# Kernel optimization log

Hardware: AMD Instinct MI355X
Metric: run time of the kernel (lower is better)

Reference implementation:

```python
import jax, jax.numpy as jnp
import numpy as np

N, T, D, E1 = 64, 32, 128, 128
EPS = 1e-6


def _mlp(x, W1, b1, W2, b2):
    # Linear -> ReLU -> (Dropout: identity in eval) -> Linear
    return jnp.maximum(x @ W1 + b1, 0.0) @ W2 + b2


def _forward(x_time, x_news,
             it_W1, it_b1, it_W2, it_b2,
             inw_W1, inw_b1, inw_W2, inw_b2,
             t2n_W1, t2n_b1, t2n_W2, t2n_b2,
             n2t_W1, n2t_b1, n2t_W2, n2t_b2,
             f_W1, f_b1, f_W2, f_b2,
             theta_t, theta_n):
    xt = x_time.reshape(-1, D)   # [NT, D]
    xn = x_news.reshape(-1, D)   # [NT, D]

    # incidence-matrix candidates, each [NT, E1]
    H_time = xt @ _mlp(xt.T, it_W1, it_b1, it_W2, it_b2)
    H_news = xn @ _mlp(xn.T, inw_W1, inw_b1, inw_W2, inw_b2)
    H_t2n = xt @ _mlp(xn.T, t2n_W1, t2n_b1, t2n_W2, t2n_b2)
    H_n2t = xn @ _mlp(xt.T, n2t_W1, n2t_b1, n2t_W2, n2t_b2)

    H = _mlp(jnp.concatenate([H_time, H_news, H_t2n, H_n2t], axis=1),
             f_W1, f_b1, f_W2, f_b2)  # [NT, E1]

    # column-wise standardization (torch.std is unbiased -> ddof=1) + softmax over nodes
    H = (H - H.mean(axis=0, keepdims=True)) / (H.std(axis=0, ddof=1, keepdims=True) + EPS)
    H = jax.nn.softmax(H, axis=0)

    # pairwise Jensen-Shannon divergence between columns of H -> [E1, E1]
    logH = jnp.log(H)
    M = (H[:, :, None] + H[:, None, :]) * 0.5          # [NT, E1, E1]
    kl_pm = jnp.sum(H[:, :, None] * (logH[:, :, None] - jnp.log(M)), axis=0)  # KL(P||M)
    # KL(Q||M)[i,j] == KL(P||M)[j,i] since M is symmetric in (i,j)
    jsd = (kl_pm + kl_pm.T) * 0.5

    jm = jsd.mean(axis=0)                               # [E1]
    njm = (jm - jm.mean()) / (jm.std(ddof=1) + EPS)
    w = jax.nn.softmax(njm)                             # diagonal of hyperedge weight W

    # Hypergraph conv with residual: x + elu(H @ diag(w) @ H.T @ x @ theta)
    # reassociated (exactly equal math) to avoid the O((NT)^2) intermediate
    Hw = H * w[None, :]                                 # [NT, E1]
    xt = xt + jax.nn.elu(Hw @ (H.T @ (xt @ theta_t)))
    xn = xn + jax.nn.elu(Hw @ (H.T @ (xn @ theta_n)))

    return xt.reshape(N, T, D), xn.reshape(N, T, D)


def setup_inputs() -> dict:
    key = jax.random.key(0)
    ks = iter(jax.random.split(key, 32))
    NT = N * T

    def lin(i, o):
        return (jax.random.normal(next(ks), (i, o), jnp.float32) / np.float32(np.sqrt(i)))

    inp = {
        "x_time": jax.random.normal(next(ks), (N, T, D), jnp.float32),
        "x_news": jax.random.normal(next(ks), (N, T, D), jnp.float32),
    }
    for pre in ["it", "inw", "t2n", "n2t"]:
        inp[pre + "_W1"] = lin(NT, E1)
        inp[pre + "_b1"] = jnp.zeros((E1,), jnp.float32)
        inp[pre + "_W2"] = lin(E1, E1)
        inp[pre + "_b2"] = jnp.zeros((E1,), jnp.float32)
    inp["f_W1"] = lin(4 * E1, E1)
    inp["f_b1"] = jnp.zeros((E1,), jnp.float32)
    inp["f_W2"] = lin(E1, E1)
    inp["f_b2"] = jnp.zeros((E1,), jnp.float32)
    # HypergraphConvolution uses torch.randn init for theta
    inp["theta_t"] = jax.random.normal(next(ks), (D, D), jnp.float32)
    inp["theta_n"] = jax.random.normal(next(ks), (D, D), jnp.float32)
    return inp


def reference(x_time, x_news,
              it_W1, it_b1, it_W2, it_b2,
              inw_W1, inw_b1, inw_W2, inw_b2,
              t2n_W1, t2n_b1, t2n_W2, t2n_b2,
              n2t_W1, n2t_b1, n2t_W2, n2t_b2,
              f_W1, f_b1, f_W2, f_b2,
              theta_t, theta_n):
    return _forward(x_time, x_news,
                    it_W1, it_b1, it_W2, it_b2,
                    inw_W1, inw_b1, inw_W2, inw_b2,
                    t2n_W1, t2n_b1, t2n_W2, t2n_b2,
                    n2t_W1, n2t_b1, n2t_W2, n2t_b2,
                    f_W1, f_b1, f_W2, f_b2,
                    theta_t, theta_n)
```

## Files before the change

### kernel.cpp

```cpp
#include <hip/hip_runtime.h>
#include <hip/hip_bf16.h>
#include <math.h>

#define NTOT 2048
#define DIM  128
#define MSPLIT 8
#define ZSPLIT 8
#define JT 16
#define JNC 128
#define JNSPLIT 8

struct P4 { const float* p[4]; };

__global__ __launch_bounds__(256) void gk_mlp1t(P4 X, P4 W1, float* __restrict__ Gs) {
  int k = blockIdx.z;
  int m0 = (blockIdx.x & 3) * 32;
  int e0 = (blockIdx.x >> 2) * 32;
  int split = blockIdx.y;
  int n0 = split * (NTOT / MSPLIT);
  const float* Xp = X.p[k];
  const float* Wp = W1.p[k];
  __shared__ float Xs[32][36], Ws[32][36];
  int tid = threadIdx.x;
  int lr = tid >> 3;
  int lc = (tid & 7) * 4;
  int tx = tid & 15, ty = tid >> 4;
  float a00 = 0.f, a01 = 0.f, a10 = 0.f, a11 = 0.f;
  long g0 = (long)(n0 + lr) * DIM;
  float4 xv = *(const float4*)(Xp + g0 + m0 + lc);
  float4 wv = *(const float4*)(Wp + g0 + e0 + lc);
  for (int nb = 0; nb < NTOT / MSPLIT; nb += 32) {
    *(float4*)&Xs[lr][lc] = xv;
    *(float4*)&Ws[lr][lc] = wv;
    __syncthreads();
    if (nb + 32 < NTOT / MSPLIT) {
      long gn = (long)(n0 + nb + 32 + lr) * DIM;
      xv = *(const float4*)(Xp + gn + m0 + lc);
      wv = *(const float4*)(Wp + gn + e0 + lc);
    }
    #pragma unroll
    for (int nn = 0; nn < 32; ++nn) {
      float x0 = Xs[nn][2*ty], x1 = Xs[nn][2*ty+1];
      float w0 = Ws[nn][2*tx], w1 = Ws[nn][2*tx+1];
      a00 += x0 * w0; a01 += x0 * w1;
      a10 += x1 * w0; a11 += x1 * w1;
    }
    __syncthreads();
  }
  float* Gk = Gs + ((long)k * MSPLIT + split) * 16384;
  int m = m0 + 2 * ty, e = e0 + 2 * tx;
  Gk[m * DIM + e]           = a00;
  Gk[m * DIM + e + 1]       = a01;
  Gk[(m + 1) * DIM + e]     = a10;
  Gk[(m + 1) * DIM + e + 1] = a11;
}

__global__ __launch_bounds__(256) void gk_mab(const float* __restrict__ Gs, P4 B1, P4 W2, P4 B2,
                                              const float* __restrict__ fW1, float* __restrict__ AB) {
  int m = blockIdx.x;
  int e = threadIdx.x & 127;
  int half = threadIdx.x >> 7;
  int k0 = half, k1 = half + 2;
  __shared__ float rk[4][DIM];
  __shared__ float mk[4][DIM];
  {
    const float* G0 = Gs + (long)k0 * MSPLIT * 16384 + m * DIM + e;
    const float* G1 = Gs + (long)k1 * MSPLIT * 16384 + m * DIM + e;
    float s0 = 0.f, s1 = 0.f;
    #pragma unroll
    for (int s = 0; s < MSPLIT; ++s) { s0 += G0[s * 16384]; s1 += G1[s * 16384]; }
    rk[k0][e] = fmaxf(s0 + B1.p[k0][e], 0.f);
    rk[k1][e] = fmaxf(s1 + B1.p[k1][e], 0.f);
  }
  __syncthreads();
  {
    const float* Wa = W2.p[k0];
    const float* Wb = W2.p[k1];
    float a0 = B2.p[k0][e], a1 = B2.p[k1][e];
    #pragma unroll 8
    for (int j = 0; j < DIM; ++j) {
      a0 += rk[k0][j] * Wa[j * DIM + e];
      a1 += rk[k1][j] * Wb[j * DIM + e];
    }
    mk[k0][e] = a0;
    mk[k1][e] = a1;
  }
  __syncthreads();
  const float* Ma = mk[half];
  const float* Mb = mk[half + 2];
  const float* W0 = fW1 + (half == 0 ? 0 : 128) * DIM;
  const float* W1p = fW1 + (half == 0 ? 256 : 384) * DIM;
  float acc = 0.f;
  #pragma unroll 8
  for (int j = 0; j < DIM; ++j)
    acc += Ma[j] * W0[j * DIM + e] + Mb[j] * W1p[j * DIM + e];
  AB[(long)half * 16384 + m * DIM + e] = acc;
}

__global__ __launch_bounds__(256) void gk_h12t(const float* __restrict__ xt, const float* __restrict__ xn,
                                               const float* __restrict__ AB, const float* __restrict__ fb1,
                                               const float* __restrict__ fW2, const float* __restrict__ fb2,
                                               float* __restrict__ HrawT) {
  int n0 = blockIdx.x * 8;
  int e  = threadIdx.x & 127;
  int rr = (threadIdx.x >> 7) << 2;
  __shared__ float stT[DIM][8], snT[DIM][8], h1T[DIM][8];
  {
    int c = threadIdx.x & 31, rq = threadIdx.x >> 5;
    const float* xtr = xt + (long)(n0 + rq) * DIM;
    const float* xnr = xn + (long)(n0 + rq) * DIM;
    #pragma unroll
    for (int i = 0; i < 4; ++i) {
      int d = c + 32 * i;
      stT[d][rq] = xtr[d];
      snT[d][rq] = xnr[d];
    }
  }
  __syncthreads();
  float4 acc1 = make_float4(0.f, 0.f, 0.f, 0.f);
  #pragma unroll 8
  for (int k = 0; k < DIM; ++k) {
    float a = AB[k * DIM + e];
    float b = AB[16384 + k * DIM + e];
    const float4 xv = *(const float4*)&stT[k][rr];
    const float4 nv = *(const float4*)&snT[k][rr];
    acc1.x += xv.x * a + nv.x * b;
    acc1.y += xv.y * a + nv.y * b;
    acc1.z += xv.z * a + nv.z * b;
    acc1.w += xv.w * a + nv.w * b;
  }
  float b1v = fb1[e];
  float4 h1;
  h1.x = fmaxf(acc1.x + b1v, 0.f);
  h1.y = fmaxf(acc1.y + b1v, 0.f);
  h1.z = fmaxf(acc1.z + b1v, 0.f);
  h1.w = fmaxf(acc1.w + b1v, 0.f);
  *(float4*)&h1T[e][rr] = h1;
  __syncthreads();
  float4 acc2 = make_float4(0.f, 0.f, 0.f, 0.f);
  #pragma unroll 8
  for (int j = 0; j < DIM; ++j) {
    float wv = fW2[j * DIM + e];
    const float4 hv = *(const float4*)&h1T[j][rr];
    acc2.x += hv.x * wv;
    acc2.y += hv.y * wv;
    acc2.z += hv.z * wv;
    acc2.w += hv.w * wv;
  }
  float b2v = fb2[e];
  float4 o;
  o.x = acc2.x + b2v; o.y = acc2.y + b2v; o.z = acc2.z + b2v; o.w = acc2.w + b2v;
  *(float4*)&HrawT[(long)e * NTOT + n0 + rr] = o;
}

__global__ __launch_bounds__(256) void colsoft_k(const float* __restrict__ HrawT,
                                                 float* __restrict__ HTp, float* __restrict__ Ecol,
                                                 float* __restrict__ Gacc) {
  int e = blockIdx.x;
  int t = threadIdx.x;
  if (e == 0 && t < DIM) Gacc[t] = 0.f;
  __shared__ float sa[4], sb[4], sc[4];
  float v[8];
  float sum = 0.f, sq = 0.f, mx = -3.4e38f;
  #pragma unroll
  for (int r = 0; r < 8; ++r) {
    float x = HrawT[(long)e * NTOT + t + 256 * r];
    v[r] = x;
    sum += x; sq += x * x; mx = fmaxf(mx, x);
  }
  #pragma unroll
  for (int o = 32; o > 0; o >>= 1) {
    sum += __shfl_down(sum, o);
    sq  += __shfl_down(sq, o);
    mx   = fmaxf(mx, __shfl_down(mx, o));
  }
  if ((t & 63) == 0) { int w = t >> 6; sa[w] = sum; sb[w] = sq; sc[w] = mx; }
  __syncthreads();
  sum = sa[0] + sa[1] + sa[2] + sa[3];
  sq  = sb[0] + sb[1] + sb[2] + sb[3];
  mx  = fmaxf(fmaxf(sc[0], sc[1]), fmaxf(sc[2], sc[3]));
  float mean = sum * (1.f / NTOT);
  float var  = (sq - sum * mean) * (1.f / (NTOT - 1));
  float ia   = 1.f / (sqrtf(fmaxf(var, 0.f)) + 1e-6f);
  float smax = (mx - mean) * ia;
  __syncthreads();

  float den = 0.f;
  #pragma unroll
  for (int r = 0; r < 8; ++r) {
    float s = (v[r] - mean) * ia - smax;
    v[r] = s;
    den += __expf(s);
  }
  #pragma unroll
  for (int o = 32; o > 0; o >>= 1) den += __shfl_down(den, o);
  if ((t & 63) == 0) sa[t >> 6] = den;
  __syncthreads();
  den = sa[0] + sa[1] + sa[2] + sa[3];
  float logden = __logf(den);
  float invden = 1.f / den;
  __syncthreads();

  float ent = 0.f;
  #pragma unroll
  for (int r = 0; r < 8; ++r) {
    float s = v[r];
    float pv = __expf(s) * invden;
    HTp[(long)e * NTOT + t + 256 * r] = pv;
    ent += pv * (s - logden);
  }
  #pragma unroll
  for (int o = 32; o > 0; o >>= 1) ent += __shfl_down(ent, o);
  if ((t & 63) == 0) sa[t >> 6] = ent;
  __syncthreads();
  if (t == 0) Ecol[e] = sa[0] + sa[1] + sa[2] + sa[3];
}

__global__ __launch_bounds__(256) void jsd_tile(const float* __restrict__ HTp,
                                                float* __restrict__ g) {
  int b = blockIdx.x;
  int bi = 0, rem = b;
  while (rem >= 8 - bi) { rem -= 8 - bi; ++bi; }
  int bj = bi + rem;
  int n0 = blockIdx.y * (NTOT / JNSPLIT);

  __shared__ float Ti[JT][JNC + 2];
  __shared__ float Tj[JT][JNC + 2];
  __shared__ float red[JT][JT + 1];

  int tid = threadIdx.x;
  int ti = tid >> 4, tj = tid & 15;
  bool active = (bi != bj) || (ti < tj);
  float acc = 0.f;

  int lc = tid >> 4;
  int ln = (tid & 15) * 8;

  for (int c = 0; c < NTOT / JNSPLIT; c += JNC) {
    const float* si = HTp + (long)(bi * JT + lc) * NTOT + n0 + c + ln;
    const float* sj = HTp + (long)(bj * JT + lc) * NTOT + n0 + c + ln;
    #pragma unroll
    for (int r = 0; r < 8; ++r) Ti[lc][ln + r] = si[r];
    #pragma unroll
    for (int r = 0; r < 8; ++r) Tj[lc][ln + r] = sj[r];
    __syncthreads();
    if (active) {
      #pragma unroll 4
      for (int n = 0; n < JNC; ++n) {
        float s = Ti[ti][n] + Tj[tj][n];
        acc += s * __logf(fmaxf(0.5f * s, 1e-38f));
      }
    }
    __syncthreads();
  }

  red[ti][tj] = active ? acc : 0.f;
  __syncthreads();
  if (tid < JT) {
    float s = 0.f;
    #pragma unroll
    for (int j = 0; j < JT; ++j) s += red[tid][j];
    atomicAdd(&g[bi * JT + tid], -s);
  } else if (tid < 2 * JT) {
    int c2 = tid - JT;
    float s = 0.f;
    #pragma unroll
    for (int i = 0; i < JT; ++i) s += red[i][c2];
    atomicAdd(&g[bj * JT + c2], -s);
  }
}

__global__ __launch_bounds__(256) void xz_k(const float* __restrict__ HTp, const float* __restrict__ xt,
                                            const float* __restrict__ xn, float* __restrict__ Xzs) {
  int bt = blockIdx.z;
  const float* x = bt ? xn : xt;
  int split = blockIdx.y;
  float* C = Xzs + ((long)bt * ZSPLIT + split) * 16384;
  int e0 = (blockIdx.x & 3) * 32, d0 = (blockIdx.x >> 2) * 32;
  int n0 = split * (NTOT / ZSPLIT);
  __shared__ float As[32][33], Bs[32][36];
  int tid = threadIdx.x, col = tid & 31, row = tid >> 5;
  int lr = tid >> 3, lc4 = (tid & 7) * 4;
  int tx = tid & 15, ty = tid >> 4;
  float a00 = 0.f, a01 = 0.f, a10 = 0.f, a11 = 0.f;
  float pa[4]; float4 pb;
  #pragma unroll
  for (int r = 0; r < 4; ++r) pa[r] = HTp[(long)(e0 + row + r * 8) * NTOT + n0 + col];
  pb = *(const float4*)(x + (long)(n0 + lr) * DIM + d0 + lc4);
  for (int nb = 0; nb < NTOT / ZSPLIT; nb += 32) {
    #pragma unroll
    for (int r = 0; r < 4; ++r) As[col][row + r * 8] = pa[r];
    *(float4*)&Bs[lr][lc4] = pb;
    __syncthreads();
    if (nb + 32 < NTOT / ZSPLIT) {
      #pragma unroll
      for (int r = 0; r < 4; ++r)
        pa[r] = HTp[(long)(e0 + row + r * 8) * NTOT + n0 + nb + 32 + col];
      pb = *(const float4*)(x + (long)(n0 + nb + 32 + lr) * DIM + d0 + lc4);
    }
    #pragma unroll
    for (int nn = 0; nn < 32; ++nn) {
      float e0v = As[nn][2*ty], e1v = As[nn][2*ty+1];
      float d0v = Bs[nn][2*tx], d1v = Bs[nn][2*tx+1];
      a00 += e0v * d0v; a01 += e0v * d1v;
      a10 += e1v * d0v; a11 += e1v * d1v;
    }
    __syncthreads();
  }
  int e = e0 + 2 * ty, d = d0 + 2 * tx;
  C[e * DIM + d]           = a00;
  C[e * DIM + d + 1]       = a01;
  C[(e + 1) * DIM + d]     = a10;
  C[(e + 1) * DIM + d + 1] = a11;
}

__global__ __launch_bounds__(128) void zs_k(const float* __restrict__ Xzs, const float* __restrict__ thT,
                                            const float* __restrict__ thN, const float* __restrict__ g,
                                            const float* __restrict__ Ecol, float* __restrict__ Zw) {
  int e = blockIdx.x, d = threadIdx.x, bt = blockIdx.y;
  __shared__ float s2[2];
  __shared__ float swv;
  int t = d;
  float ec = Ecol[t];
  float v = ec;
  #pragma unroll
  for (int o = 32; o > 0; o >>= 1) v += __shfl_down(v, o);
  if ((t & 63) == 0) s2[t >> 6] = v;
  __syncthreads();
  float S = s2[0] + s2[1];
  __syncthreads();
  float jm = (g[t] + 126.f * ec + S) * (1.0f / 256.0f);
  v = jm;
  #pragma unroll
  for (int o = 32; o > 0; o >>= 1) v += __shfl_down(v, o);
  if ((t & 63) == 0) s2[t >> 6] = v;
  __syncthreads();
  float mean = (s2[0] + s2[1]) * (1.0f / 128.0f);
  __syncthreads();
  float dv = jm - mean;
  v = dv * dv;
  #pragma unroll
  for (int o = 32; o > 0; o >>= 1) v += __shfl_down(v, o);
  if ((t & 63) == 0) s2[t >> 6] = v;
  __syncthreads();
  float var = (s2[0] + s2[1]) * (1.0f / 127.0f);
  float njm = dv / (sqrtf(var) + 1e-6f);
  __syncthreads();
  v = njm;
  #pragma unroll
  for (int o = 32; o > 0; o >>= 1) v = fmaxf(v, __shfl_down(v, o));
  if ((t & 63) == 0) s2[t >> 6] = v;
  __syncthreads();
  float mx = fmaxf(s2[0], s2[1]);
  float ex = __expf(njm - mx);
  __syncthreads();
  v = ex;
  #pragma unroll
  for (int o = 32; o > 0; o >>= 1) v += __shfl_down(v, o);
  if ((t & 63) == 0) s2[t >> 6] = v;
  __syncthreads();
  if (t == e) swv = ex / (s2[0] + s2[1]);
  __syncthreads();
  float we = swv;

  const float* src = Xzs + (long)bt * ZSPLIT * 16384 + e * DIM + d;
  const float* th = bt ? thN : thT;
  __shared__ float s[DIM];
  float xv = 0.f;
  #pragma unroll
  for (int sp = 0; sp < ZSPLIT; ++sp) xv += src[sp * 16384];
  s[d] = xv;
  __syncthreads();
  float acc = 0.f;
  #pragma unroll 8
  for (int k = 0; k < DIM; ++k) acc += s[k] * th[(long)k * DIM + d];
  Zw[bt * 16384 + e * DIM + d] = acc * we;
}

__global__ __launch_bounds__(256) void uk_t(const float* __restrict__ HTp, const float* __restrict__ Zw,
                                            const float* __restrict__ xt, const float* __restrict__ xn,
                                            float* __restrict__ out) {
  int bt = blockIdx.z;
  const float* x = bt ? xn : xt;
  const float* B = Zw + bt * 16384;
  float* o = out + (long)bt * NTOT * DIM;
  int d0 = blockIdx.x * 32, n0 = blockIdx.y * 32;
  __shared__ float As[32][33], Bs[32][36];
  int tid = threadIdx.x, col = tid & 31, row = tid >> 5;
  int lr = tid >> 3, lc4 = (tid & 7) * 4;
  int tx = tid & 15, ty = tid >> 4;
  float a00 = 0.f, a01 = 0.f, a10 = 0.f, a11 = 0.f;
  float pa[4]; float4 pb;
  #pragma unroll
  for (int r = 0; r < 4; ++r) pa[r] = HTp[(long)(row + r * 8) * NTOT + n0 + col];
  pb = *(const float4*)(B + (long)lr * DIM + d0 + lc4);
  for (int eb = 0; eb < DIM; eb += 32) {
    #pragma unroll
    for (int r = 0; r < 4; ++r) As[col][row + r * 8] = pa[r];
    *(float4*)&Bs[lr][lc4] = pb;
    __syncthreads();
    if (eb + 32 < DIM) {
      #pragma unroll
      for (int r = 0; r < 4; ++r)
        pa[r] = HTp[(long)(eb + 32 + row + r * 8) * NTOT + n0 + col];
      pb = *(const float4*)(B + (long)(eb + 32 + lr) * DIM + d0 + lc4);
    }
    #pragma unroll
    for (int ee = 0; ee < 32; ++ee) {
      float x0 = As[2*ty][ee], x1 = As[2*ty+1][ee];
      float b0 = Bs[ee][2*tx], b1 = Bs[ee][2*tx+1];
      a00 += x0 * b0; a01 += x0 * b1;
      a10 += x1 * b0; a11 += x1 * b1;
    }
    __syncthreads();
  }
  int n = n0 + 2 * ty, d = d0 + 2 * tx;
  long i0 = (long)n * DIM + d, i1 = i0 + DIM;
  float e00 = a00 > 0.f ? a00 : expm1f(a00);
  float e01 = a01 > 0.f ? a01 : expm1f(a01);
  float e10 = a10 > 0.f ? a10 : expm1f(a10);
  float e11 = a11 > 0.f ? a11 : expm1f(a11);
  o[i0]     = x[i0]     + e00;
  o[i0 + 1] = x[i0 + 1] + e01;
  o[i1]     = x[i1]     + e10;
  o[i1 + 1] = x[i1 + 1] + e11;
}

extern "C" void kernel_launch(void* const* d_in, const int* in_sizes, int n_in,
                              void* d_out, int out_size, void* d_ws, size_t ws_size,
                              hipStream_t stream) {
  const float* xt = (const float*)d_in[0];
  const float* xn = (const float*)d_in[1];
  const float *W1[4], *b1[4], *W2[4], *b2[4];
  for (int k = 0; k < 4; ++k) {
    W1[k] = (const float*)d_in[2 + 4*k];
    b1[k] = (const float*)d_in[3 + 4*k];
    W2[k] = (const float*)d_in[4 + 4*k];
    b2[k] = (const float*)d_in[5 + 4*k];
  }
  const float* fW1 = (const float*)d_in[18];
  const float* fb1 = (const float*)d_in[19];
  const float* fW2 = (const float*)d_in[20];
  const float* fb2 = (const float*)d_in[21];
  const float* thT = (const float*)d_in[22];
  const float* thN = (const float*)d_in[23];

  float* ws    = (float*)d_ws;
  float* Gacc  = ws;
  float* Ecol  = ws + 128;
  float* Zw    = ws + 384;
  float* Xzs   = ws + 33152;
  float* Gs    = ws + 295296;
  float* AB    = ws + 885120;
  float* HrawT = ws + 917888;
  float* HTp   = ws + 1180032;

  float* out = (float*)d_out;

  P4 Xs  = {{xt, xn, xn, xt}};
  P4 W1s = {{W1[0], W1[1], W1[2], W1[3]}};
  P4 B1s = {{b1[0], b1[1], b1[2], b1[3]}};
  P4 W2s = {{W2[0], W2[1], W2[2], W2[3]}};
  P4 B2s = {{b2[0], b2[1], b2[2], b2[3]}};

  gk_mlp1t<<<dim3(16, MSPLIT, 4), 256, 0, stream>>>(Xs, W1s, Gs);
  gk_mab  <<<128, 256, 0, stream>>>(Gs, B1s, W2s, B2s, fW1, AB);
  gk_h12t <<<256, 256, 0, stream>>>(xt, xn, AB, fb1, fW2, fb2, HrawT);

  colsoft_k<<<DIM, 256, 0, stream>>>(HrawT, HTp, Ecol, Gacc);

  jsd_tile<<<dim3(36, JNSPLIT), 256, 0, stream>>>(HTp, Gacc);

  xz_k<<<dim3(16, ZSPLIT, 2), 256, 0, stream>>>(HTp, xt, xn, Xzs);
  zs_k<<<dim3(128, 2), 128, 0, stream>>>(Xzs, thT, thN, Gacc, Ecol, Zw);
  uk_t<<<dim3(4, 64, 2), 256, 0, stream>>>(HTp, Zw, xt, xn, out);

  (void)in_sizes; (void)n_in; (void)out_size; (void)ws_size;
}
```

Measured before the change: 183.8 us.

## Fuse all pipeline stages into one cooperative persistent kernel with grid syncs

Replaces the eight separate kernel launches with a single cooperative kernel of 512 blocks that runs every stage in sequence and separates the stages with grid-wide barriers. Stage work is remapped onto the fixed block count, which doubles the JSD and Xz split factors and halves the per-block rows in the H projection. The aim is to remove per-launch overhead and the gaps between the many small dependent kernels. In exchange, grid.sync costs are added, and stages with fewer tiles than blocks leave some blocks idle. The design also depends on all 512 blocks fitting at once, which launch_bounds(256,2) is meant to allow.

Measured after the change: 527.2 us. 187% more time.

```diff
diff --git a/kernel.cpp b/kernel.cpp
--- a/kernel.cpp
+++ b/kernel.cpp
@@ -1,429 +1,413 @@
 #include <hip/hip_runtime.h>
-#include <hip/hip_bf16.h>
+#include <hip/hip_cooperative_groups.h>
 #include <math.h>
+
+namespace cg = cooperative_groups;
 
 #define NTOT 2048
 #define DIM  128
 #define MSPLIT 8
-#define ZSPLIT 8
+#define ZSPLIT 16
 #define JT 16
 #define JNC 128
-#define JNSPLIT 8
-
-struct P4 { const float* p[4]; };
-
-__global__ __launch_bounds__(256) void gk_mlp1t(P4 X, P4 W1, float* __restrict__ Gs) {
-  int k = blockIdx.z;
-  int m0 = (blockIdx.x & 3) * 32;
-  int e0 = (blockIdx.x >> 2) * 32;
-  int split = blockIdx.y;
-  int n0 = split * (NTOT / MSPLIT);
-  const float* Xp = X.p[k];
-  const float* Wp = W1.p[k];
-  __shared__ float Xs[32][36], Ws[32][36];
-  int tid = threadIdx.x;
-  int lr = tid >> 3;
-  int lc = (tid & 7) * 4;
-  int tx = tid & 15, ty = tid >> 4;
-  float a00 = 0.f, a01 = 0.f, a10 = 0.f, a11 = 0.f;
-  long g0 = (long)(n0 + lr) * DIM;
-  float4 xv = *(const float4*)(Xp + g0 + m0 + lc);
-  float4 wv = *(const float4*)(Wp + g0 + e0 + lc);
-  for (int nb = 0; nb < NTOT / MSPLIT; nb += 32) {
-    *(float4*)&Xs[lr][lc] = xv;
-    *(float4*)&Ws[lr][lc] = wv;
-    __syncthreads();
-    if (nb + 32 < NTOT / MSPLIT) {
-      long gn = (long)(n0 + nb + 32 + lr) * DIM;
-      xv = *(const float4*)(Xp + gn + m0 + lc);
-      wv = *(const float4*)(Wp + gn + e0 + lc);
-    }
-    #pragma unroll
-    for (int nn = 0; nn < 32; ++nn) {
-      float x0 = Xs[nn][2*ty], x1 = Xs[nn][2*ty+1];
-      float w0 = Ws[nn][2*tx], w1 = Ws[nn][2*tx+1];
-      a00 += x0 * w0; a01 += x0 * w1;
-      a10 += x1 * w0; a11 += x1 * w1;
-    }
-    __syncthreads();
-  }
-  float* Gk = Gs + ((long)k * MSPLIT + split) * 16384;
-  int m = m0 + 2 * ty, e = e0 + 2 * tx;
-  Gk[m * DIM + e]           = a00;
-  Gk[m * DIM + e + 1]       = a01;
-  Gk[(m + 1) * DIM + e]     = a10;
-  Gk[(m + 1) * DIM + e + 1] = a11;
-}
-
-__global__ __launch_bounds__(256) void gk_mab(const float* __restrict__ Gs, P4 B1, P4 W2, P4 B2,
-                                              const float* __restrict__ fW1, float* __restrict__ AB) {
-  int m = blockIdx.x;
-  int e = threadIdx.x & 127;
-  int half = threadIdx.x >> 7;
-  int k0 = half, k1 = half + 2;
-  __shared__ float rk[4][DIM];
-  __shared__ float mk[4][DIM];
-  {
-    const float* G0 = Gs + (long)k0 * MSPLIT * 16384 + m * DIM + e;
-    const float* G1 = Gs + (long)k1 * MSPLIT * 16384 + m * DIM + e;
-    float s0 = 0.f, s1 = 0.f;
-    #pragma unroll
-    for (int s = 0; s < MSPLIT; ++s) { s0 += G0[s * 16384]; s1 += G1[s * 16384]; }
-    rk[k0][e] = fmaxf(s0 + B1.p[k0][e], 0.f);
-    rk[k1][e] = fmaxf(s1 + B1.p[k1][e], 0.f);
-  }
-  __syncthreads();
-  {
-    const float* Wa = W2.p[k0];
-    const float* Wb = W2.p[k1];
-    float a0 = B2.p[k0][e], a1 = B2.p[k1][e];
-    #pragma unroll 8
-    for (int j = 0; j < DIM; ++j) {
-      a0 += rk[k0][j] * Wa[j * DIM + e];
-      a1 += rk[k1][j] * Wb[j * DIM + e];
-    }
-    mk[k0][e] = a0;
-    mk[k1][e] = a1;
-  }
-  __syncthreads();
-  const float* Ma = mk[half];
-  const float* Mb = mk[half + 2];
-  const float* W0 = fW1 + (half == 0 ? 0 : 128) * DIM;
-  const float* W1p = fW1 + (half == 0 ? 256 : 384) * DIM;
-  float acc = 0.f;
-  #pragma unroll 8
-  for (int j = 0; j < DIM; ++j)
-    acc += Ma[j] * W0[j * DIM + e] + Mb[j] * W1p[j * DIM + e];
-  AB[(long)half * 16384 + m * DIM + e] = acc;
-}
-
-__global__ __launch_bounds__(256) void gk_h12t(const float* __restrict__ xt, const float* __restrict__ xn,
-                                               const float* __restrict__ AB, const float* __restrict__ fb1,
-                                               const float* __restrict__ fW2, const float* __restrict__ fb2,
-                                               float* __restrict__ HrawT) {
-  int n0 = blockIdx.x * 8;
-  int e  = threadIdx.x & 127;
-  int rr = (threadIdx.x >> 7) << 2;
-  __shared__ float stT[DIM][8], snT[DIM][8], h1T[DIM][8];
-  {
-    int c = threadIdx.x & 31, rq = threadIdx.x >> 5;
-    const float* xtr = xt + (long)(n0 + rq) * DIM;
-    const float* xnr = xn + (long)(n0 + rq) * DIM;
-    #pragma unroll
-    for (int i = 0; i < 4; ++i) {
-      int d = c + 32 * i;
-      stT[d][rq] = xtr[d];
-      snT[d][rq] = xnr[d];
-    }
-  }
-  __syncthreads();
-  float4 acc1 = make_float4(0.f, 0.f, 0.f, 0.f);
-  #pragma unroll 8
-  for (int k = 0; k < DIM; ++k) {
-    float a = AB[k * DIM + e];
-    float b = AB[16384 + k * DIM + e];
-    const float4 xv = *(const float4*)&stT[k][rr];
-    const float4 nv = *(const float4*)&snT[k][rr];
-    acc1.x += xv.x * a + nv.x * b;
-    acc1.y += xv.y * a + nv.y * b;
-    acc1.z += xv.z * a + nv.z * b;
-    acc1.w += xv.w * a + nv.w * b;
-  }
-  float b1v = fb1[e];
-  float4 h1;
-  h1.x = fmaxf(acc1.x + b1v, 0.f);
-  h1.y = fmaxf(acc1.y + b1v, 0.f);
-  h1.z = fmaxf(acc1.z + b1v, 0.f);
-  h1.w = fmaxf(acc1.w + b1v, 0.f);
-  *(float4*)&h1T[e][rr] = h1;
-  __syncthreads();
-  float4 acc2 = make_float4(0.f, 0.f, 0.f, 0.f);
-  #pragma unroll 8
-  for (int j = 0; j < DIM; ++j) {
-    float wv = fW2[j * DIM + e];
-    const float4 hv = *(const float4*)&h1T[j][rr];
-    acc2.x += hv.x * wv;
-    acc2.y += hv.y * wv;
-    acc2.z += hv.z * wv;
-    acc2.w += hv.w * wv;
-  }
-  float b2v = fb2[e];
-  float4 o;
-  o.x = acc2.x + b2v; o.y = acc2.y + b2v; o.z = acc2.z + b2v; o.w = acc2.w + b2v;
-  *(float4*)&HrawT[(long)e * NTOT + n0 + rr] = o;
-}
-
-__global__ __launch_bounds__(256) void colsoft_k(const float* __restrict__ HrawT,
-                                                 float* __restrict__ HTp, float* __restrict__ Ecol,
-                                                 float* __restrict__ Gacc) {
-  int e = blockIdx.x;
-  int t = threadIdx.x;
-  if (e == 0 && t < DIM) Gacc[t] = 0.f;
-  __shared__ float sa[4], sb[4], sc[4];
-  float v[8];
-  float sum = 0.f, sq = 0.f, mx = -3.4e38f;
-  #pragma unroll
-  for (int r = 0; r < 8; ++r) {
-    float x = HrawT[(long)e * NTOT + t + 256 * r];
-    v[r] = x;
-    sum += x; sq += x * x; mx = fmaxf(mx, x);
-  }
-  #pragma unroll
-  for (int o = 32; o > 0; o >>= 1) {
-    sum += __shfl_down(sum, o);
-    sq  += __shfl_down(sq, o);
-    mx   = fmaxf(mx, __shfl_down(mx, o));
-  }
-  if ((t & 63) == 0) { int w = t >> 6; sa[w] = sum; sb[w] = sq; sc[w] = mx; }
-  __syncthreads();
-  sum = sa[0] + sa[1] + sa[2] + sa[3];
-  sq  = sb[0] + sb[1] + sb[2] + sb[3];
-  mx  = fmaxf(fmaxf(sc[0], sc[1]), fmaxf(sc[2], sc[3]));
-  float mean = sum * (1.f / NTOT);
-  float var  = (sq - sum * mean) * (1.f / (NTOT - 1));
-  float ia   = 1.f / (sqrtf(fmaxf(var, 0.f)) + 1e-6f);
-  float smax = (mx - mean) * ia;
-  __syncthreads();
-
-  float den = 0.f;
-  #pragma unroll
-  for (int r = 0; r < 8; ++r) {
-    float s = (v[r] - mean) * ia - smax;
-    v[r] = s;
-    den += __expf(s);
-  }
-  #pragma unroll
-  for (int o = 32; o > 0; o >>= 1) den += __shfl_down(den, o);
-  if ((t & 63) == 0) sa[t >> 6] = den;
-  __syncthreads();
-  den = sa[0] + sa[1] + sa[2] + sa[3];
-  float logden = __logf(den);
-  float invden = 1.f / den;
-  __syncthreads();
-
-  float ent = 0.f;
-  #pragma unroll
-  for (int r = 0; r < 8; ++r) {
-    float s = v[r];
-    float pv = __expf(s) * invden;
-    HTp[(long)e * NTOT + t + 256 * r] = pv;
-    ent += pv * (s - logden);
-  }
-  #pragma unroll
-  for (int o = 32; o > 0; o >>= 1) ent += __shfl_down(ent, o);
-  if ((t & 63) == 0) sa[t >> 6] = ent;
-  __syncthreads();
-  if (t == 0) Ecol[e] = sa[0] + sa[1] + sa[2] + sa[3];
-}
-
-__global__ __launch_bounds__(256) void jsd_tile(const float* __restrict__ HTp,
-                                                float* __restrict__ g) {
-  int b = blockIdx.x;
+#define JNSPLIT 16
+#define NBLK 512
+
+struct KArgs {
+  const float* X[4];
+  const float* W1[4]; const float* B1[4];
+  const float* W2[4]; const float* B2[4];
+  const float *xt, *xn, *fW1, *fb1, *fW2, *fb2, *thT, *thN;
+  float *Gacc, *Ecol, *Zw, *Xzs, *Gs, *AB, *HrawT, *HTp, *out;
+};
+
+struct SMem {
+  union {
+    struct { float Xs[32][36], Ws[32][36]; } g1;
+    struct { float rk[4][DIM], mk[4][DIM]; } g2;
+    struct { float xT[DIM][4], nT[DIM][4], h1[DIM][4]; } g3;
+    struct { float sa[4], sb[4], sc[4]; } g4;
+    struct { float Ti[JT][JNC + 2], Tj[JT][JNC + 2], red[JT][JT + 1]; } g5;
+    struct { float As[32][33], Bs[32][36]; } g6;
+    struct { float s[DIM]; } g7;
+  };
+};
+
+__device__ __forceinline__ void jsd_body(SMem& sm, int j, const KArgs& A) {
+  int b = j % 36, ny = j / 36;
   int bi = 0, rem = b;
   while (rem >= 8 - bi) { rem -= 8 - bi; ++bi; }
   int bj = bi + rem;
-  int n0 = blockIdx.y * (NTOT / JNSPLIT);
-
-  __shared__ float Ti[JT][JNC + 2];
-  __shared__ float Tj[JT][JNC + 2];
-  __shared__ float red[JT][JT + 1];
-
+  int n0 = ny * (NTOT / JNSPLIT);
   int tid = threadIdx.x;
   int ti = tid >> 4, tj = tid & 15;
   bool active = (bi != bj) || (ti < tj);
+  int lc = tid >> 4, ln = (tid & 15) * 8;
+  __syncthreads();
+  const float* si = A.HTp + (long)(bi * JT + lc) * NTOT + n0 + ln;
+  const float* sj = A.HTp + (long)(bj * JT + lc) * NTOT + n0 + ln;
+  #pragma unroll
+  for (int r = 0; r < 8; ++r) sm.g5.Ti[lc][ln + r] = si[r];
+  #pragma unroll
+  for (int r = 0; r < 8; ++r) sm.g5.Tj[lc][ln + r] = sj[r];
+  __syncthreads();
   float acc = 0.f;
-
-  int lc = tid >> 4;
-  int ln = (tid & 15) * 8;
-
-  for (int c = 0; c < NTOT / JNSPLIT; c += JNC) {
-    const float* si = HTp + (long)(bi * JT + lc) * NTOT + n0 + c + ln;
-    const float* sj = HTp + (long)(bj * JT + lc) * NTOT + n0 + c + ln;
-    #pragma unroll
-    for (int r = 0; r < 8; ++r) Ti[lc][ln + r] = si[r];
-    #pragma unroll
-    for (int r = 0; r < 8; ++r) Tj[lc][ln + r] = sj[r];
-    __syncthreads();
-    if (active) {
-      #pragma unroll 4
-      for (int n = 0; n < JNC; ++n) {
-        float s = Ti[ti][n] + Tj[tj][n];
-        acc += s * __logf(fmaxf(0.5f * s, 1e-38f));
-      }
-    }
-    __syncthreads();
-  }
-
-  red[ti][tj] = active ? acc : 0.f;
+  if (active) {
+    #pragma unroll 4
+    for (int n = 0; n < JNC; ++n) {
+      float s = sm.g5.Ti[ti][n] + sm.g5.Tj[tj][n];
+      acc += s * __logf(fmaxf(0.5f * s, 1e-38f));
+    }
+  }
+  sm.g5.red[ti][tj] = active ? acc : 0.f;
   __syncthreads();
   if (tid < JT) {
     float s = 0.f;
     #pragma unroll
-    for (int j = 0; j < JT; ++j) s += red[tid][j];
-    atomicAdd(&g[bi * JT + tid], -s);
+    for (int q = 0; q < JT; ++q) s += sm.g5.red[tid][q];
+    atomicAdd(&A.Gacc[bi * JT + tid], -s);
   } else if (tid < 2 * JT) {
     int c2 = tid - JT;
     float s = 0.f;
     #pragma unroll
-    for (int i = 0; i < JT; ++i) s += red[i][c2];
-    atomicAdd(&g[bj * JT + c2], -s);
+    for (int i = 0; i < JT; ++i) s += sm.g5.red[i][c2];
+    atomicAdd(&A.Gacc[bj * JT + c2], -s);
   }
 }
 
-__global__ __launch_bounds__(256) void xz_k(const float* __restrict__ HTp, const float* __restrict__ xt,
-                                            const float* __restrict__ xn, float* __restrict__ Xzs) {
-  int bt = blockIdx.z;
-  const float* x = bt ? xn : xt;
-  int split = blockIdx.y;
-  float* C = Xzs + ((long)bt * ZSPLIT + split) * 16384;
-  int e0 = (blockIdx.x & 3) * 32, d0 = (blockIdx.x >> 2) * 32;
-  int n0 = split * (NTOT / ZSPLIT);
-  __shared__ float As[32][33], Bs[32][36];
-  int tid = threadIdx.x, col = tid & 31, row = tid >> 5;
-  int lr = tid >> 3, lc4 = (tid & 7) * 4;
-  int tx = tid & 15, ty = tid >> 4;
-  float a00 = 0.f, a01 = 0.f, a10 = 0.f, a11 = 0.f;
-  float pa[4]; float4 pb;
-  #pragma unroll
-  for (int r = 0; r < 4; ++r) pa[r] = HTp[(long)(e0 + row + r * 8) * NTOT + n0 + col];
-  pb = *(const float4*)(x + (long)(n0 + lr) * DIM + d0 + lc4);
-  for (int nb = 0; nb < NTOT / ZSPLIT; nb += 32) {
-    #pragma unroll
-    for (int r = 0; r < 4; ++r) As[col][row + r * 8] = pa[r];
-    *(float4*)&Bs[lr][lc4] = pb;
-    __syncthreads();
-    if (nb + 32 < NTOT / ZSPLIT) {
-      #pragma unroll
-      for (int r = 0; r < 4; ++r)
-        pa[r] = HTp[(long)(e0 + row + r * 8) * NTOT + n0 + nb + 32 + col];
-      pb = *(const float4*)(x + (long)(n0 + nb + 32 + lr) * DIM + d0 + lc4);
-    }
-    #pragma unroll
-    for (int nn = 0; nn < 32; ++nn) {
-      float e0v = As[nn][2*ty], e1v = As[nn][2*ty+1];
-      float d0v = Bs[nn][2*tx], d1v = Bs[nn][2*tx+1];
-      a00 += e0v * d0v; a01 += e0v * d1v;
-      a10 += e1v * d0v; a11 += e1v * d1v;
-    }
-    __syncthreads();
-  }
-  int e = e0 + 2 * ty, d = d0 + 2 * tx;
-  C[e * DIM + d]           = a00;
-  C[e * DIM + d + 1]       = a01;
-  C[(e + 1) * DIM + d]     = a10;
-  C[(e + 1) * DIM + d + 1] = a11;
-}
-
-__global__ __launch_bounds__(128) void zs_k(const float* __restrict__ Xzs, const float* __restrict__ thT,
-                                            const float* __restrict__ thN, const float* __restrict__ g,
-                                            const float* __restrict__ Ecol, float* __restrict__ Zw) {
-  int e = blockIdx.x, d = threadIdx.x, bt = blockIdx.y;
-  __shared__ float s2[2];
-  __shared__ float swv;
-  int t = d;
-  float ec = Ecol[t];
-  float v = ec;
-  #pragma unroll
-  for (int o = 32; o > 0; o >>= 1) v += __shfl_down(v, o);
-  if ((t & 63) == 0) s2[t >> 6] = v;
+__global__ __launch_bounds__(256, 2) void mega(KArgs A) {
+  cg::grid_group grid = cg::this_grid();
+  __shared__ SMem sm;
+  const int bid = blockIdx.x;
+  const int tid = threadIdx.x;
+
+  {
+    int k = bid >> 7, t16 = bid & 15, split = (bid >> 4) & 7;
+    int m0 = (t16 & 3) * 32, e0 = (t16 >> 2) * 32;
+    int n0 = split * (NTOT / MSPLIT);
+    const float* Xp = A.X[k];
+    const float* Wp = A.W1[k];
+    int lr = tid >> 3, lc = (tid & 7) * 4;
+    int tx = tid & 15, ty = tid >> 4;
+    float a00 = 0.f, a01 = 0.f, a10 = 0.f, a11 = 0.f;
+    long g0 = (long)(n0 + lr) * DIM;
+    float4 xv = *(const float4*)(Xp + g0 + m0 + lc);
+    float4 wv = *(const float4*)(Wp + g0 + e0 + lc);
+    for (int nb = 0; nb < NTOT / MSPLIT; nb += 32) {
+      *(float4*)&sm.g1.Xs[lr][lc] = xv;
+      *(float4*)&sm.g1.Ws[lr][lc] = wv;
+      __syncthreads();
+      if (nb + 32 < NTOT / MSPLIT) {
+        long gn = (long)(n0 + nb + 32 + lr) * DIM;
+        xv = *(const float4*)(Xp + gn + m0 + lc);
+        wv = *(const float4*)(Wp + gn + e0 + lc);
+      }
+      #pragma unroll
+      for (int nn = 0; nn < 32; ++nn) {
+        float x0 = sm.g1.Xs[nn][2*ty], x1 = sm.g1.Xs[nn][2*ty+1];
+        float w0 = sm.g1.Ws[nn][2*tx], w1 = sm.g1.Ws[nn][2*tx+1];
+        a00 += x0 * w0; a01 += x0 * w1;
+        a10 += x1 * w0; a11 += x1 * w1;
+      }
+      __syncthreads();
+    }
+    float* Gk = A.Gs + ((long)k * MSPLIT + split) * 16384;
+    int m = m0 + 2 * ty, e = e0 + 2 * tx;
+    Gk[m * DIM + e]           = a00;
+    Gk[m * DIM + e + 1]       = a01;
+    Gk[(m + 1) * DIM + e]     = a10;
+    Gk[(m + 1) * DIM + e + 1] = a11;
+  }
+  grid.sync();
+
+  if (bid < 128) {
+    int m = bid;
+    int e = tid & 127;
+    int half = tid >> 7;
+    int k0 = half, k1 = half + 2;
+    {
+      const float* G0 = A.Gs + (long)k0 * MSPLIT * 16384 + m * DIM + e;
+      const float* G1 = A.Gs + (long)k1 * MSPLIT * 16384 + m * DIM + e;
+      float s0 = 0.f, s1 = 0.f;
+      #pragma unroll
+      for (int s = 0; s < MSPLIT; ++s) { s0 += G0[s * 16384]; s1 += G1[s * 16384]; }
+      sm.g2.rk[k0][e] = fmaxf(s0 + A.B1[k0][e], 0.f);
+      sm.g2.rk[k1][e] = fmaxf(s1 + A.B1[k1][e], 0.f);
+    }
+    __syncthreads();
+    {
+      const float* Wa = A.W2[k0];
+      const float* Wb = A.W2[k1];
+      float a0 = A.B2[k0][e], a1 = A.B2[k1][e];
+      #pragma unroll 8
+      for (int j = 0; j < DIM; ++j) {
+        a0 += sm.g2.rk[k0][j] * Wa[j * DIM + e];
+        a1 += sm.g2.rk[k1][j] * Wb[j * DIM + e];
+      }
+      sm.g2.mk[k0][e] = a0;
+      sm.g2.mk[k1][e] = a1;
+    }
+    __syncthreads();
+    const float* Ma = sm.g2.mk[half];
+    const float* Mb = sm.g2.mk[half + 2];
+    const float* W0 = A.fW1 + (half == 0 ? 0 : 128) * DIM;
+    const float* W1p = A.fW1 + (half == 0 ? 256 : 384) * DIM;
+    float acc = 0.f;
+    #pragma unroll 8
+    for (int j = 0; j < DIM; ++j)
+      acc += Ma[j] * W0[j * DIM + e] + Mb[j] * W1p[j * DIM + e];
+    A.AB[(long)half * 16384 + m * DIM + e] = acc;
+  }
+  grid.sync();
+
+  {
+    int n0 = bid * 4;
+    int e = tid & 127;
+    int half = tid >> 7;
+    {
+      int c = tid & 31, rq = tid >> 5;
+      const float* src = (rq < 4) ? (A.xt + (long)(n0 + rq) * DIM)
+                                  : (A.xn + (long)(n0 + rq - 4) * DIM);
+      float (*dst)[4] = (rq < 4) ? sm.g3.xT : sm.g3.nT;
+      int rr = rq & 3;
+      #pragma unroll
+      for (int i = 0; i < 4; ++i) {
+        int d = c + 32 * i;
+        dst[d][rr] = src[d];
+      }
+    }
+    __syncthreads();
+    float2 acc1 = make_float2(0.f, 0.f);
+    #pragma unroll 8
+    for (int k = 0; k < DIM; ++k) {
+      float a = A.AB[k * DIM + e];
+      float b = A.AB[16384 + k * DIM + e];
+      float2 xv = *(const float2*)&sm.g3.xT[k][half * 2];
+      float2 nv = *(const float2*)&sm.g3.nT[k][half * 2];
+      acc1.x += xv.x * a + nv.x * b;
+      acc1.y += xv.y * a + nv.y * b;
+    }
+    float b1v = A.fb1[e];
+    float2 h1 = make_float2(fmaxf(acc1.x + b1v, 0.f), fmaxf(acc1.y + b1v, 0.f));
+    *(float2*)&sm.g3.h1[e][half * 2] = h1;
+    __syncthreads();
+    float2 acc2 = make_float2(0.f, 0.f);
+    #pragma unroll 8
+    for (int j = 0; j < DIM; ++j) {
+      float wv = A.fW2[j * DIM + e];
+      float2 hv = *(const float2*)&sm.g3.h1[j][half * 2];
+      acc2.x += hv.x * wv;
+      acc2.y += hv.y * wv;
+    }
+    float b2v = A.fb2[e];
+    float2 o = make_float2(acc2.x + b2v, acc2.y + b2v);
+    *(float2*)&A.HrawT[(long)e * NTOT + n0 + half * 2] = o;
+  }
+  grid.sync();
+
+  if (bid < DIM) {
+    int e = bid;
+    int t = tid;
+    float v[8];
+    float sum = 0.f, sq = 0.f, mx = -3.4e38f;
+    #pragma unroll
+    for (int r = 0; r < 8; ++r) {
+      float x = A.HrawT[(long)e * NTOT + t + 256 * r];
+      v[r] = x;
+      sum += x; sq += x * x; mx = fmaxf(mx, x);
+    }
+    #pragma unroll
+    for (int o = 32; o > 0; o >>= 1) {
+      sum += __shfl_down(sum, o);
+      sq  += __shfl_down(sq, o);
+      mx   = fmaxf(mx, __shfl_down(mx, o));
+    }
+    if ((t & 63) == 0) { int w = t >> 6; sm.g4.sa[w] = sum; sm.g4.sb[w] = sq; sm.g4.sc[w] = mx; }
+    __syncthreads();
+    sum = sm.g4.sa[0] + sm.g4.sa[1] + sm.g4.sa[2] + sm.g4.sa[3];
+    sq  = sm.g4.sb[0] + sm.g4.sb[1] + sm.g4.sb[2] + sm.g4.sb[3];
+    mx  = fmaxf(fmaxf(sm.g4.sc[0], sm.g4.sc[1]), fmaxf(sm.g4.sc[2], sm.g4.sc[3]));
+    float mean = sum * (1.f / NTOT);
+    float var  = (sq - sum * mean) * (1.f / (NTOT - 1));
+    float ia   = 1.f / (sqrtf(fmaxf(var, 0.f)) + 1e-6f);
+    float smax = (mx - mean) * ia;
+    __syncthreads();
+
+    float den = 0.f;
+    #pragma unroll
+    for (int r = 0; r < 8; ++r) {
+      float s = (v[r] - mean) * ia - smax;
+      v[r] = s;
+      den += __expf(s);
+    }
+    #pragma unroll
+    for (int o = 32; o > 0; o >>= 1) den += __shfl_down(den, o);
+    if ((t & 63) == 0) sm.g4.sa[t >> 6] = den;
+    __syncthreads();
+    den = sm.g4.sa[0] + sm.g4.sa[1] + sm.g4.sa[2] + sm.g4.sa[3];
+    float logden = __logf(den);
+    float invden = 1.f / den;
+    __syncthreads();
+
+    float ent = 0.f;
+    #pragma unroll
+    for (int r = 0; r < 8; ++r) {
+      float s = v[r];
+      float pv = __expf(s) * invden;
+      A.HTp[(long)e * NTOT + t + 256 * r] = pv;
+      ent += pv * (s - logden);
+    }
+    #pragma unroll
+    for (int o = 32; o > 0; o >>= 1) ent += __shfl_down(ent, o);
+    if ((t & 63) == 0) sm.g4.sa[t >> 6] = ent;
+    __syncthreads();
+    if (t == 0) A.Ecol[e] = sm.g4.sa[0] + sm.g4.sa[1] + sm.g4.sa[2] + sm.g4.sa[3];
+  } else if (bid == DIM) {
+    if (tid < DIM) A.Gacc[tid] = 0.f;
+  }
+  grid.sync();
+
+  jsd_body(sm, bid, A);
+  if (bid < 576 - NBLK) jsd_body(sm, NBLK + bid, A);
+
   __syncthreads();
-  float S = s2[0] + s2[1];
-  __syncthreads();
-  float jm = (g[t] + 126.f * ec + S) * (1.0f / 256.0f);
-  v = jm;
-  #pragma unroll
-  for (int o = 32; o > 0; o >>= 1) v += __shfl_down(v, o);
-  if ((t & 63) == 0) s2[t >> 6] = v;
-  __syncthreads();
-  float mean = (s2[0] + s2[1]) * (1.0f / 128.0f);
-  __syncthreads();
-  float dv = jm - mean;
-  v = dv * dv;
-  #pragma unroll
-  for (int o = 32; o > 0; o >>= 1) v += __shfl_down(v, o);
-  if ((t & 63) == 0) s2[t >> 6] = v;
-  __syncthreads();
-  float var = (s2[0] + s2[1]) * (1.0f / 127.0f);
-  float njm = dv / (sqrtf(var) + 1e-6f);
-  __syncthreads();
-  v = njm;
-  #pragma unroll
-  for (int o = 32; o > 0; o >>= 1) v = fmaxf(v, __shfl_down(v, o));
-  if ((t & 63) == 0) s2[t >> 6] = v;
-  __syncthreads();
-  float mx = fmaxf(s2[0], s2[1]);
-  float ex = __expf(njm - mx);
-  __syncthreads();
-  v = ex;
-  #pragma unroll
-  for (int o = 32; o > 0; o >>= 1) v += __shfl_down(v, o);
-  if ((t & 63) == 0) s2[t >> 6] = v;
-  __syncthreads();
-  if (t == e) swv = ex / (s2[0] + s2[1]);
-  __syncthreads();
-  float we = swv;
-
-  const float* src = Xzs + (long)bt * ZSPLIT * 16384 + e * DIM + d;
-  const float* th = bt ? thN : thT;
-  __shared__ float s[DIM];
-  float xv = 0.f;
-  #pragma unroll
-  for (int sp = 0; sp < ZSPLIT; ++sp) xv += src[sp * 16384];
-  s[d] = xv;
-  __syncthreads();
-  float acc = 0.f;
-  #pragma unroll 8
-  for (int k = 0; k < DIM; ++k) acc += s[k] * th[(long)k * DIM + d];
-  Zw[bt * 16384 + e * DIM + d] = acc * we;
-}
-
-__global__ __launch_bounds__(256) void uk_t(const float* __restrict__ HTp, const float* __restrict__ Zw,
-                                            const float* __restrict__ xt, const float* __restrict__ xn,
-                                            float* __restrict__ out) {
-  int bt = blockIdx.z;
-  const float* x = bt ? xn : xt;
-  const float* B = Zw + bt * 16384;
-  float* o = out + (long)bt * NTOT * DIM;
-  int d0 = blockIdx.x * 32, n0 = blockIdx.y * 32;
-  __shared__ float As[32][33], Bs[32][36];
-  int tid = threadIdx.x, col = tid & 31, row = tid >> 5;
-  int lr = tid >> 3, lc4 = (tid & 7) * 4;
-  int tx = tid & 15, ty = tid >> 4;
-  float a00 = 0.f, a01 = 0.f, a10 = 0.f, a11 = 0.f;
-  float pa[4]; float4 pb;
-  #pragma unroll
-  for (int r = 0; r < 4; ++r) pa[r] = HTp[(long)(row + r * 8) * NTOT + n0 + col];
-  pb = *(const float4*)(B + (long)lr * DIM + d0 + lc4);
-  for (int eb = 0; eb < DIM; eb += 32) {
-    #pragma unroll
-    for (int r = 0; r < 4; ++r) As[col][row + r * 8] = pa[r];
-    *(float4*)&Bs[lr][lc4] = pb;
-    __syncthreads();
-    if (eb + 32 < DIM) {
-      #pragma unroll
-      for (int r = 0; r < 4; ++r)
-        pa[r] = HTp[(long)(eb + 32 + row + r * 8) * NTOT + n0 + col];
-      pb = *(const float4*)(B + (long)(eb + 32 + lr) * DIM + d0 + lc4);
-    }
-    #pragma unroll
-    for (int ee = 0; ee < 32; ++ee) {
-      float x0 = As[2*ty][ee], x1 = As[2*ty+1][ee];
-      float b0 = Bs[ee][2*tx], b1 = Bs[ee][2*tx+1];
-      a00 += x0 * b0; a01 += x0 * b1;
-      a10 += x1 * b0; a11 += x1 * b1;
-    }
-    __syncthreads();
-  }
-  int n = n0 + 2 * ty, d = d0 + 2 * tx;
-  long i0 = (long)n * DIM + d, i1 = i0 + DIM;
-  float e00 = a00 > 0.f ? a00 : expm1f(a00);
-  float e01 = a01 > 0.f ? a01 : expm1f(a01);
-  float e10 = a10 > 0.f ? a10 : expm1f(a10);
-  float e11 = a11 > 0.f ? a11 : expm1f(a11);
-  o[i0]     = x[i0]     + e00;
-  o[i0 + 1] = x[i0 + 1] + e01;
-  o[i1]     = x[i1]     + e10;
-  o[i1 + 1] = x[i1 + 1] + e11;
+  {
+    int bt = bid >> 8;
+    int split = (bid >> 4) & 15;
+    int t16 = bid & 15;
+    const float* x = bt ? A.xn : A.xt;
+    float* C = A.Xzs + ((long)bt * ZSPLIT + split) * 16384;
+    int e0 = (t16 & 3) * 32, d0 = (t16 >> 2) * 32;
+    int n0 = split * (NTOT / ZSPLIT);
+    int col = tid & 31, row = tid >> 5;
+    int lr = tid >> 3, lc4 = (tid & 7) * 4;
+    int tx = tid & 15, ty = tid >> 4;
+    float a00 = 0.f, a01 = 0.f, a10 = 0.f, a11 = 0.f;
+    float pa[4]; float4 pb;
+    #pragma unroll
+    for (int r = 0; r < 4; ++r) pa[r] = A.HTp[(long)(e0 + row + r * 8) * NTOT + n0 + col];
+    pb = *(const float4*)(x + (long)(n0 + lr) * DIM + d0 + lc4);
+    for (int nb = 0; nb < NTOT / ZSPLIT; nb += 32) {
+      #pragma unroll
+      for (int r = 0; r < 4; ++r) sm.g6.As[col][row + r * 8] = pa[r];
+      *(float4*)&sm.g6.Bs[lr][lc4] = pb;
+      __syncthreads();
+      if (nb + 32 < NTOT / ZSPLIT) {
+        #pragma unroll
+        for (int r = 0; r < 4; ++r)
+          pa[r] = A.HTp[(long)(e0 + row + r * 8) * NTOT + n0 + nb + 32 + col];
+        pb = *(const float4*)(x + (long)(n0 + nb + 32 + lr) * DIM + d0 + lc4);
+      }
+      #pragma unroll
+      for (int nn = 0; nn < 32; ++nn) {
+        float e0v = sm.g6.As[nn][2*ty], e1v = sm.g6.As[nn][2*ty+1];
+        float d0v = sm.g6.Bs[nn][2*tx], d1v = sm.g6.Bs[nn][2*tx+1];
+        a00 += e0v * d0v; a01 += e0v * d1v;
+        a10 += e1v * d0v; a11 += e1v * d1v;
+      }
+      __syncthreads();
+    }
+    int e = e0 + 2 * ty, d = d0 + 2 * tx;
+    C[e * DIM + d]           = a00;
+    C[e * DIM + d + 1]       = a01;
+    C[(e + 1) * DIM + d]     = a10;
+    C[(e + 1) * DIM + d + 1] = a11;
+  }
+  grid.sync();
+
+  if (bid < 256) {
+    int e = bid & 127, bt = bid >> 7;
+    int d = tid & 127;
+    float we;
+    {
+      int l = tid & 63;
+      float gA = A.Gacc[l], gB = A.Gacc[l + 64];
+      float eA = A.Ecol[l], eB = A.Ecol[l + 64];
+      float S = eA + eB;
+      #pragma unroll
+      for (int o = 32; o > 0; o >>= 1) S += __shfl_xor(S, o);
+      float jA = (gA + 126.f * eA + S) * (1.f / 256.f);
+      float jB = (gB + 126.f * eB + S) * (1.f / 256.f);
+      float sn = jA + jB;
+      #pragma unroll
+      for (int o = 32; o > 0; o >>= 1) sn += __shfl_xor(sn, o);
+      float mean = sn * (1.f / 128.f);
+      float dA = jA - mean, dB = jB - mean;
+      float q = dA * dA + dB * dB;
+      #pragma unroll
+      for (int o = 32; o > 0; o >>= 1) q += __shfl_xor(q, o);
+      float inv = 1.f / (sqrtf(q * (1.f / 127.f)) + 1e-6f);
+      float nA = dA * inv, nB = dB * inv;
+      float mx = fmaxf(nA, nB);
+      #pragma unroll
+      for (int o = 32; o > 0; o >>= 1) mx = fmaxf(mx, __shfl_xor(mx, o));
+      float xA = __expf(nA - mx), xB = __expf(nB - mx);
+      float den = xA + xB;
+      #pragma unroll
+      for (int o = 32; o > 0; o >>= 1) den += __shfl_xor(den, o);
+      float sel = (e < 64) ? nA : nB;
+      float ne = __shfl(sel, e & 63);
+      we = __expf(ne - mx) / den;
+    }
+    const float* src = A.Xzs + (long)bt * ZSPLIT * 16384 + e * DIM + d;
+    float xv = 0.f;
+    #pragma unroll
+    for (int sp = 0; sp < ZSPLIT; ++sp) xv += src[sp * 16384];
+    if (tid < 128) sm.g7.s[d] = xv;
+    __syncthreads();
+    const float* th = bt ? A.thN : A.thT;
+    float acc = 0.f;
+    #pragma unroll 8
+    for (int k = 0; k < DIM; ++k) acc += sm.g7.s[k] * th[(long)k * DIM + d];
+    if (tid < 128) A.Zw[bt * 16384 + e * DIM + d] = acc * we;
+  }
+  grid.sync();
+
+  {
+    int bt = bid >> 8;
+    const float* x = bt ? A.xn : A.xt;
+    const float* B = A.Zw + bt * 16384;
+    float* o = A.out + (long)bt * NTOT * DIM;
+    int d0 = (bid & 3) * 32, n0 = ((bid >> 2) & 63) * 32;
+    int col = tid & 31, row = tid >> 5;
+    int lr = tid >> 3, lc4 = (tid & 7) * 4;
+    int tx = tid & 15, ty = tid >> 4;
+    float a00 = 0.f, a01 = 0.f, a10 = 0.f, a11 = 0.f;
+    float pa[4]; float4 pb;
+    #pragma unroll
+    for (int r = 0; r < 4; ++r) pa[r] = A.HTp[(long)(row + r * 8) * NTOT + n0 + col];
+    pb = *(const float4*)(B + (long)lr * DIM + d0 + lc4);
+    for (int eb = 0; eb < DIM; eb += 32) {
+      #pragma unroll
+      for (int r = 0; r < 4; ++r) sm.g6.As[col][row + r * 8] = pa[r];
+      *(float4*)&sm.g6.Bs[lr][lc4] = pb;
+      __syncthreads();
+      if (eb + 32 < DIM) {
+        #pragma unroll
+        for (int r = 0; r < 4; ++r)
+          pa[r] = A.HTp[(long)(eb + 32 + row + r * 8) * NTOT + n0 + col];
+        pb = *(const float4*)(B + (long)(eb + 32 + lr) * DIM + d0 + lc4);
+      }
+      #pragma unroll
+      for (int ee = 0; ee < 32; ++ee) {
+        float x0 = sm.g6.As[2*ty][ee], x1 = sm.g6.As[2*ty+1][ee];
+        float b0 = sm.g6.Bs[ee][2*tx], b1 = sm.g6.Bs[ee][2*tx+1];
+        a00 += x0 * b0; a01 += x0 * b1;
+        a10 += x1 * b0; a11 += x1 * b1;
+      }
+      __syncthreads();
+    }
+    int n = n0 + 2 * ty, d = d0 + 2 * tx;
+    long i0 = (long)n * DIM + d, i1 = i0 + DIM;
+    float e00 = a00 > 0.f ? a00 : expm1f(a00);
+    float e01 = a01 > 0.f ? a01 : expm1f(a01);
+    float e10 = a10 > 0.f ? a10 : expm1f(a10);
+    float e11 = a11 > 0.f ? a11 : expm1f(a11);
+    o[i0]     = x[i0]     + e00;
+    o[i0 + 1] = x[i0 + 1] + e01;
+    o[i1]     = x[i1]     + e10;
+    o[i1 + 1] = x[i1 + 1] + e11;
+  }
 }
 
 extern "C" void kernel_launch(void* const* d_in, const int* in_sizes, int n_in,
@@ -431,49 +415,36 @@
                               hipStream_t stream) {
   const float* xt = (const float*)d_in[0];
   const float* xn = (const float*)d_in[1];
-  const float *W1[4], *b1[4], *W2[4], *b2[4];
+
+  KArgs A;
+  A.X[0] = xt; A.X[1] = xn; A.X[2] = xn; A.X[3] = xt;
   for (int k = 0; k < 4; ++k) {
-    W1[k] = (const float*)d_in[2 + 4*k];
-    b1[k] = (const float*)d_in[3 + 4*k];
-    W2[k] = (const float*)d_in[4 + 4*k];
-    b2[k] = (const float*)d_in[5 + 4*k];
-  }
-  const float* fW1 = (const float*)d_in[18];
-  const float* fb1 = (const float*)d_in[19];
-  const float* fW2 = (const float*)d_in[20];
-  const float* fb2 = (const float*)d_in[21];
-  const float* thT = (const float*)d_in[22];
-  const float* thN = (const float*)d_in[23];
-
-  float* ws    = (float*)d_ws;
-  float* Gacc  = ws;
-  float* Ecol  = ws + 128;
-  float* Zw    = ws + 384;
-  float* Xzs   = ws + 33152;
-  float* Gs    = ws + 295296;
-  float* AB    = ws + 885120;
-  float* HrawT = ws + 917888;
-  float* HTp   = ws + 1180032;
-
-  float* out = (float*)d_out;
-
-  P4 Xs  = {{xt, xn, xn, xt}};
-  P4 W1s = {{W1[0], W1[1], W1[2], W1[3]}};
-  P4 B1s = {{b1[0], b1[1], b1[2], b1[3]}};
-  P4 W2s = {{W2[0], W2[1], W2[2], W2[3]}};
-  P4 B2s = {{b2[0], b2[1], b2[2], b2[3]}};
-
-  gk_mlp1t<<<dim3(16, MSPLIT, 4), 256, 0, stream>>>(Xs, W1s, Gs);
-  gk_mab  <<<128, 256, 0, stream>>>(Gs, B1s, W2s, B2s, fW1, AB);
-  gk_h12t <<<256, 256, 0, stream>>>(xt, xn, AB, fb1, fW2, fb2, HrawT);
-
-  colsoft_k<<<DIM, 256, 0, stream>>>(HrawT, HTp, Ecol, Gacc);
-
-  jsd_tile<<<dim3(36, JNSPLIT), 256, 0, stream>>>(HTp, Gacc);
-
-  xz_k<<<dim3(16, ZSPLIT, 2), 256, 0, stream>>>(HTp, xt, xn, Xzs);
-  zs_k<<<dim3(128, 2), 128, 0, stream>>>(Xzs, thT, thN, Gacc, Ecol, Zw);
-  uk_t<<<dim3(4, 64, 2), 256, 0, stream>>>(HTp, Zw, xt, xn, out);
+    A.W1[k] = (const float*)d_in[2 + 4*k];
+    A.B1[k] = (const float*)d_in[3 + 4*k];
+    A.W2[k] = (const float*)d_in[4 + 4*k];
+    A.B2[k] = (const float*)d_in[5 + 4*k];
+  }
+  A.xt = xt; A.xn = xn;
+  A.fW1 = (const float*)d_in[18];
+  A.fb1 = (const float*)d_in[19];
+  A.fW2 = (const float*)d_in[20];
+  A.fb2 = (const float*)d_in[21];
+  A.thT = (const float*)d_in[22];
+  A.thN = (const float*)d_in[23];
+
+  float* ws = (float*)d_ws;
+  A.Gacc  = ws;
+  A.Ecol  = ws + 128;
+  A.Zw    = ws + 384;
+  A.Xzs   = ws + 33152;
+  A.Gs    = A.Xzs + 2 * ZSPLIT * 16384;
+  A.AB    = A.Gs + 4 * MSPLIT * 16384;
+  A.HrawT = A.AB + 2 * 16384;
+  A.HTp   = A.HrawT + (long)NTOT * DIM;
+  A.out   = (float*)d_out;
+
+  void* kargs[] = { (void*)&A };
+  hipLaunchCooperativeKernel((void*)mega, dim3(NBLK), dim3(256), kargs, 0, stream);
 
   (void)in_sizes; (void)n_in; (void)out_size; (void)ws_size;
 }
```
